# Performance work log

Hardware: AMD Instinct MI355X
Metric: run time of the kernel (lower is better)

The kernel has to match this reference:

```python
import jax, jax.numpy as jnp
import numpy as np

B, S, D, H, DK = 2, 2048, 1024, 16, 64  # d_model = n_heads * d_k

def setup_inputs() -> dict:
    key = jax.random.key(0)
    ks = jax.random.split(key, 11)
    s = 1.0 / np.sqrt(D)
    return {
        "Q": jax.random.normal(ks[0], (B, S, D), jnp.float32),
        "K": jax.random.normal(ks[1], (B, S, D), jnp.float32),
        "V": jax.random.normal(ks[2], (B, S, D), jnp.float32),
        "wq": jax.random.normal(ks[3], (D, D), jnp.float32) * s,
        "bq": jnp.zeros((D,), jnp.float32),
        "wk": jax.random.normal(ks[4], (D, D), jnp.float32) * s,
        "bk": jnp.zeros((D,), jnp.float32),
        "wv": jax.random.normal(ks[5], (D, D), jnp.float32) * s,
        "bv": jnp.zeros((D,), jnp.float32),
        "wo": jax.random.normal(ks[6], (D, D), jnp.float32) * s,
        "bo": jnp.zeros((D,), jnp.float32),
    }

def reference(Q, K, V, wq, bq, wk, bk, wv, bv, wo, bo):
    # linear projections (torch Linear: x @ W^T + b)
    q = Q @ wq.T + bq
    k = K @ wk.T + bk
    v = V @ wv.T + bv
    # split heads -> [B, H, S, DK]
    def split(t):
        return t.reshape(B, S, H, DK).transpose(0, 2, 1, 3)
    q, k, v = split(q), split(k), split(v)
    scale = 1.0 / np.sqrt(DK)
    scores = jnp.einsum('bhqd,bhkd->bhqk', q, k) * scale  # [B,H,S,S]
    probs = jax.nn.softmax(scores, axis=-1)
    # dropout is identity in eval mode
    ctx = jnp.einsum('bhqk,bhkd->bhqd', probs, v)  # [B,H,S,DK]
    ctx = ctx.transpose(0, 2, 1, 3).reshape(B, S, D)
    return ctx @ wo.T + bo
```

## Files before the change

kernel.cpp:

```cpp
#include <hip/hip_runtime.h>

#define S_LEN 2048
#define DMODEL 1024
#define DHEAD 64

typedef _Float16 half8 __attribute__((ext_vector_type(8)));
typedef _Float16 half4 __attribute__((ext_vector_type(4)));
typedef float f32x4 __attribute__((ext_vector_type(4)));
typedef int i32x4 __attribute__((ext_vector_type(4)));

#define LOG2E 1.4426950408889634f

__device__ __forceinline__ void async_copy16(const void* g, void* l) {
  __builtin_amdgcn_global_load_lds((__attribute__((address_space(1))) const void*)g,
                                   (__attribute__((address_space(3))) void*)l,
                                   16, 0, 0);
}

__device__ __forceinline__ void stage16_cvt(const float* __restrict__ gp, _Float16* lp) {
  float4 f0 = ((const float4*)gp)[0];
  float4 f1 = ((const float4*)gp)[1];
  float4 f2 = ((const float4*)gp)[2];
  float4 f3 = ((const float4*)gp)[3];
  half8 h0, h1;
  h0[0] = (_Float16)f0.x; h0[1] = (_Float16)f0.y; h0[2] = (_Float16)f0.z; h0[3] = (_Float16)f0.w;
  h0[4] = (_Float16)f1.x; h0[5] = (_Float16)f1.y; h0[6] = (_Float16)f1.z; h0[7] = (_Float16)f1.w;
  h1[0] = (_Float16)f2.x; h1[1] = (_Float16)f2.y; h1[2] = (_Float16)f2.z; h1[3] = (_Float16)f2.w;
  h1[4] = (_Float16)f3.x; h1[5] = (_Float16)f3.y; h1[6] = (_Float16)f3.z; h1[7] = (_Float16)f3.w;
  *(half8*)lp = h0;
  *(half8*)(lp + 8) = h1;
}

__global__ __launch_bounds__(256) void convert_w(const float* __restrict__ wq,
                                                 const float* __restrict__ wk,
                                                 const float* __restrict__ wv,
                                                 _Float16* __restrict__ dst) {
  const float* src = (blockIdx.y == 0) ? wq : (blockIdx.y == 1) ? wk : wv;
  _Float16* d = dst + (size_t)blockIdx.y * (DMODEL * DMODEL);
  int i = (blockIdx.x * 256 + threadIdx.x) * 4;
  float4 v = *(const float4*)(src + i);
  half4 h;
  h[0] = (_Float16)v.x; h[1] = (_Float16)v.y;
  h[2] = (_Float16)v.z; h[3] = (_Float16)v.w;
  *(half4*)(d + i) = h;
}

__global__ __launch_bounds__(256) void convert_wo(const float* __restrict__ wo,
                                                  _Float16* __restrict__ dst) {
  int i = (blockIdx.x * 256 + threadIdx.x) * 4;
  float4 v = *(const float4*)(wo + i);
  half4 h;
  h[0] = (_Float16)v.x; h[1] = (_Float16)v.y;
  h[2] = (_Float16)v.z; h[3] = (_Float16)v.w;
  *(half4*)(dst + i) = h;
}

__global__ __launch_bounds__(256) void qkv_gemm(
    const float* __restrict__ Qf, const float* __restrict__ Kf, const float* __restrict__ Vf,
    const _Float16* __restrict__ wh,
    const float* __restrict__ bq, const float* __restrict__ bk, const float* __restrict__ bv,
    _Float16* __restrict__ qo, _Float16* __restrict__ ko, _Float16* __restrict__ vt) {
  __shared__ __align__(16) _Float16 As[128 * 32];
  __shared__ __align__(16) _Float16 Bs[128 * 32];
  const int tid = threadIdx.x;
  const int wave = tid >> 6, lane = tid & 63;
  const int m15 = lane & 15, quad = lane >> 4;
  const int m0 = blockIdx.x * 128;
  const int gn0 = blockIdx.y * 128;
  const int sel = gn0 >> 10;
  const int n0 = gn0 & 1023;
  const float* Ag = (sel == 0) ? Qf : (sel == 1) ? Kf : Vf;
  const _Float16* Wg = wh + (size_t)sel * (DMODEL * DMODEL);
  const float* bias = (sel == 0) ? bq : (sel == 1) ? bk : bv;

  const int wm = (wave & 1) * 64, wn = (wave >> 1) * 64;
  const int sr = tid >> 1, sc16 = (tid & 1) * 16;

  f32x4 acc[4][4];
#pragma unroll
  for (int i = 0; i < 4; i++)
#pragma unroll
    for (int j = 0; j < 4; j++) {
      f32x4 z = {0.f, 0.f, 0.f, 0.f};
      acc[i][j] = z;
    }

  for (int k0 = 0; k0 < DMODEL; k0 += 32) {
#pragma unroll
    for (int p = 0; p < 2; p++) {
      int e = p * 2048 + tid * 8;
      async_copy16(Wg + (size_t)(n0 + (e >> 5)) * DMODEL + k0 + (e & 31),
                   (char*)Bs + p * 4096 + wave * 1024);
    }
    stage16_cvt(Ag + (size_t)(m0 + sr) * DMODEL + k0 + sc16, &As[sr * 32 + sc16]);
    __syncthreads();
    half8 af[4], bf[4];
#pragma unroll
    for (int i = 0; i < 4; i++)
      af[i] = *(const half8*)&As[(wm + i * 16 + m15) * 32 + quad * 8];
#pragma unroll
    for (int j = 0; j < 4; j++)
      bf[j] = *(const half8*)&Bs[(wn + j * 16 + m15) * 32 + quad * 8];
#pragma unroll
    for (int i = 0; i < 4; i++)
#pragma unroll
      for (int j = 0; j < 4; j++)
        acc[i][j] = __builtin_amdgcn_mfma_f32_16x16x32_f16(af[i], bf[j], acc[i][j], 0, 0, 0);
    __syncthreads();
  }
  if (sel != 2) {
    _Float16* outp = (sel == 0) ? qo : ko;
    const float scale = (sel == 0) ? (0.125f * LOG2E) : 1.0f;
#pragma unroll
    for (int i = 0; i < 4; i++) {
#pragma unroll
      for (int j = 0; j < 4; j++) {
        int gn = n0 + wn + j * 16 + m15;
        float bb = bias[gn];
#pragma unroll
        for (int r = 0; r < 4; r++) {
          int gm = m0 + wm + i * 16 + quad * 4 + r;
          outp[(size_t)gm * DMODEL + gn] = (_Float16)((acc[i][j][r] + bb) * scale);
        }
      }
    }
  } else {
#pragma unroll
    for (int i = 0; i < 4; i++) {
      int gm0 = m0 + wm + i * 16 + quad * 4;
      int b = gm0 >> 11, s = gm0 & 2047;
#pragma unroll
      for (int j = 0; j < 4; j++) {
        int gn = n0 + wn + j * 16 + m15;
        int h = gn >> 6, dk = gn & 63;
        float bb = bias[gn];
        half4 hv;
        hv[0] = (_Float16)(acc[i][j][0] + bb);
        hv[1] = (_Float16)(acc[i][j][1] + bb);
        hv[2] = (_Float16)(acc[i][j][2] + bb);
        hv[3] = (_Float16)(acc[i][j][3] + bb);
        *(half4*)(vt + ((size_t)(b * 16 + h) * 64 + dk) * 2048 + s) = hv;
      }
    }
  }
}

__global__ __launch_bounds__(256) void attn_kernel(const _Float16* __restrict__ qh,
                                                   const _Float16* __restrict__ kh,
                                                   const _Float16* __restrict__ vt,
                                                   _Float16* __restrict__ ctx) {
  __shared__ __align__(16) _Float16 Ks[2][64 * 64];
  __shared__ __align__(16) _Float16 Vs[2][64 * 64];
  const int tid = threadIdx.x;
  const int wave = tid >> 6, lane = tid & 63;
  const int m15 = lane & 15, qd = lane >> 4;
  const int q0 = blockIdx.x * 64;
  const int h = blockIdx.y, b = blockIdx.z;
  const size_t base = (size_t)b * S_LEN * DMODEL + (size_t)h * DHEAD;
  const size_t vbase = (size_t)(b * 16 + h) * 64 * 2048;

  const int qrow = q0 + wave * 16 + m15;
  half8 qf0 = *(const half8*)(qh + base + (size_t)qrow * DMODEL + qd * 8);
  half8 qf1 = *(const half8*)(qh + base + (size_t)qrow * DMODEL + 32 + qd * 8);

  const int l8 = lane >> 3, s8 = lane & 7;
  const int swz = (s8 ^ l8) * 8;
  const _Float16* ksrc = kh + base + (size_t)(wave * 8 + l8) * DMODEL + swz;
  const _Float16* vsrc = vt + vbase + (size_t)(wave * 8 + l8) * S_LEN + swz;
  char* kdst = (char*)&Ks[0][0] + wave * 1024;
  char* vdst = (char*)&Vs[0][0] + wave * 1024;

  const int kcol0 = ((qd ^ (m15 & 7)) << 4);

  f32x4 acc[4];
#pragma unroll
  for (int i = 0; i < 4; i++) { f32x4 z = {0.f, 0.f, 0.f, 0.f}; acc[i] = z; }
  float lsum = 0.f;

#pragma unroll
  for (int p = 0; p < 2; p++) {
    async_copy16(ksrc + (size_t)(p * 32) * DMODEL, kdst + p * 4096);
    async_copy16(vsrc + (size_t)(p * 32) * S_LEN, vdst + p * 4096);
  }
  __syncthreads();

  for (int it = 0; it < 32; it++) {
    const int buf = it & 1;
    if (it < 31) {
      const int kv = (it + 1) * 64;
#pragma unroll
      for (int p = 0; p < 2; p++) {
        async_copy16(ksrc + (size_t)(kv + p * 32) * DMODEL, kdst + (buf ^ 1) * 8192 + p * 4096);
        async_copy16(vsrc + (size_t)(p * 32) * S_LEN + kv, vdst + (buf ^ 1) * 8192 + p * 4096);
      }
    }
    const char* kb = (const char*)&Ks[buf][0];
    const char* vb = (const char*)&Vs[buf][0];

    f32x4 sc[4];
#pragma unroll
    for (int t = 0; t < 4; t++) {
      half8 kf0 = *(const half8*)(kb + (t * 16 + m15) * 128 + kcol0);
      half8 kf1 = *(const half8*)(kb + (t * 16 + m15) * 128 + (kcol0 ^ 64));
      f32x4 z = {0.f, 0.f, 0.f, 0.f};
      sc[t] = __builtin_amdgcn_mfma_f32_16x16x32_f16(kf0, qf0, z, 0, 0, 0);
      sc[t] = __builtin_amdgcn_mfma_f32_16x16x32_f16(kf1, qf1, sc[t], 0, 0, 0);
    }

    int pk[4][2];
#pragma unroll
    for (int t = 0; t < 4; t++) {
      float e0 = exp2f(sc[t][0]);
      float e1 = exp2f(sc[t][1]);
      float e2 = exp2f(sc[t][2]);
      float e3 = exp2f(sc[t][3]);
      lsum += (e0 + e1) + (e2 + e3);
      pk[t][0] = __builtin_bit_cast(int, __builtin_amdgcn_cvt_pkrtz(e0, e1));
      pk[t][1] = __builtin_bit_cast(int, __builtin_amdgcn_cvt_pkrtz(e2, e3));
    }

    i32x4 fh[2];
#pragma unroll
    for (int t1 = 0; t1 < 2; t1++) {
#pragma unroll
      for (int p = 0; p < 2; p++) {
        auto s1 = __builtin_amdgcn_permlane32_swap(pk[2 * t1][p], pk[2 * t1 + 1][p], false, false);
        auto s2 = __builtin_amdgcn_permlane16_swap(s1[0], s1[1], false, false);
        fh[t1][p] = (int)s2[0];
        fh[t1][2 + p] = (int)s2[1];
      }
    }
    half8 pA = __builtin_bit_cast(half8, fh[0]);
    half8 pB = __builtin_bit_cast(half8, fh[1]);

#pragma unroll
    for (int td = 0; td < 4; td++) {
      half8 vf0 = *(const half8*)(vb + (td * 16 + m15) * 128 + kcol0);
      half8 vf1 = *(const half8*)(vb + (td * 16 + m15) * 128 + (kcol0 ^ 64));
      acc[td] = __builtin_amdgcn_mfma_f32_16x16x32_f16(vf0, pA, acc[td], 0, 0, 0);
      acc[td] = __builtin_amdgcn_mfma_f32_16x16x32_f16(vf1, pB, acc[td], 0, 0, 0);
    }
    __syncthreads();
  }

  lsum += __shfl_xor(lsum, 16);
  lsum += __shfl_xor(lsum, 32);
  const float inv = 1.0f / lsum;

#pragma unroll
  for (int td = 0; td < 4; td++) {
    half4 hv;
#pragma unroll
    for (int r = 0; r < 4; r++) hv[r] = (_Float16)(acc[td][r] * inv);
    *(half4*)(ctx + base + (size_t)qrow * DMODEL + td * 16 + qd * 4) = hv;
  }
}

__global__ __launch_bounds__(256) void out_gemm(const _Float16* __restrict__ ch,
                                                const _Float16* __restrict__ who,
                                                const float* __restrict__ bo,
                                                float* __restrict__ out) {
  __shared__ __align__(16) _Float16 As[128 * 32];
  __shared__ __align__(16) _Float16 Bs[128 * 32];
  const int tid = threadIdx.x;
  const int wave = tid >> 6, lane = tid & 63;
  const int m15 = lane & 15, quad = lane >> 4;
  const int m0 = blockIdx.x * 128, n0 = blockIdx.y * 128;
  const int wm = (wave & 1) * 64, wn = (wave >> 1) * 64;

  f32x4 acc[4][4];
#pragma unroll
  for (int i = 0; i < 4; i++)
#pragma unroll
    for (int j = 0; j < 4; j++) {
      f32x4 z = {0.f, 0.f, 0.f, 0.f};
      acc[i][j] = z;
    }

  for (int k0 = 0; k0 < DMODEL; k0 += 32) {
#pragma unroll
    for (int p = 0; p < 2; p++) {
      int e = p * 2048 + tid * 8;
      async_copy16(ch + (size_t)(m0 + (e >> 5)) * DMODEL + k0 + (e & 31),
                   (char*)As + p * 4096 + wave * 1024);
      async_copy16(who + (size_t)(n0 + (e >> 5)) * DMODEL + k0 + (e & 31),
                   (char*)Bs + p * 4096 + wave * 1024);
    }
    __syncthreads();
    half8 af[4], bf[4];
#pragma unroll
    for (int i = 0; i < 4; i++)
      af[i] = *(const half8*)&As[(wm + i * 16 + m15) * 32 + quad * 8];
#pragma unroll
    for (int j = 0; j < 4; j++)
      bf[j] = *(const half8*)&Bs[(wn + j * 16 + m15) * 32 + quad * 8];
#pragma unroll
    for (int i = 0; i < 4; i++)
#pragma unroll
      for (int j = 0; j < 4; j++)
        acc[i][j] = __builtin_amdgcn_mfma_f32_16x16x32_f16(af[i], bf[j], acc[i][j], 0, 0, 0);
    __syncthreads();
  }
#pragma unroll
  for (int i = 0; i < 4; i++) {
#pragma unroll
    for (int j = 0; j < 4; j++) {
      int gn = n0 + wn + j * 16 + m15;
      float bb = bo[gn];
#pragma unroll
      for (int r = 0; r < 4; r++) {
        int gm = m0 + wm + i * 16 + quad * 4 + r;
        out[(size_t)gm * DMODEL + gn] = acc[i][j][r] + bb;
      }
    }
  }
}

extern "C" void kernel_launch(void* const* d_in, const int* in_sizes, int n_in,
                              void* d_out, int out_size, void* d_ws, size_t ws_size,
                              hipStream_t stream) {
  (void)in_sizes; (void)n_in; (void)out_size; (void)ws_size;
  const float* Q  = (const float*)d_in[0];
  const float* K  = (const float*)d_in[1];
  const float* V  = (const float*)d_in[2];
  const float* wq = (const float*)d_in[3];
  const float* bq = (const float*)d_in[4];
  const float* wk = (const float*)d_in[5];
  const float* bk = (const float*)d_in[6];
  const float* wv = (const float*)d_in[7];
  const float* bv = (const float*)d_in[8];
  const float* wo = (const float*)d_in[9];
  const float* bo = (const float*)d_in[10];
  float* out = (float*)d_out;

  _Float16* qh = (_Float16*)d_out;
  _Float16* kh = qh + (size_t)4194304;
  _Float16* vt = (_Float16*)d_ws;
  _Float16* wh = vt + (size_t)4194304;
  _Float16* ch = vt + (size_t)4194304;
  _Float16* who = (_Float16*)d_ws;

  convert_w<<<dim3(1024, 3), 256, 0, stream>>>(wq, wk, wv, wh);
  qkv_gemm<<<dim3(32, 24), 256, 0, stream>>>(Q, K, V, wh, bq, bk, bv, qh, kh, vt);
  attn_kernel<<<dim3(32, 16, 2), 256, 0, stream>>>(qh, kh, vt, ch);
  convert_wo<<<dim3(1024), 256, 0, stream>>>(wo, who);
  out_gemm<<<dim3(32, 8), 256, 0, stream>>>(ch, who, bo, out);
}
```

Baseline: 258.8 us.

## Split attention KV tile across waves instead of query rows, reduce via LDS

The attention kernel now has each wave own 16 keys of every 64-key tile across all 64 query rows, rather than owning 16 query rows across all keys. Each wave reads one K fragment per tile and uses 16x16x16 MFMAs for the PV product on locally produced probabilities. This removes the permlane shuffles and cuts redundant K/V LDS reads. The cost is a serialized cross-wave reduction of partial outputs and row sums through shared memory, with four barriers at the end, plus four times the accumulator registers. It also switches to the raw exp2 builtin.

```diff
diff --git a/kernel.cpp b/kernel.cpp
--- a/kernel.cpp
+++ b/kernel.cpp
@@ -7,7 +7,7 @@
 typedef _Float16 half8 __attribute__((ext_vector_type(8)));
 typedef _Float16 half4 __attribute__((ext_vector_type(4)));
 typedef float f32x4 __attribute__((ext_vector_type(4)));
-typedef int i32x4 __attribute__((ext_vector_type(4)));
+typedef int i32x2 __attribute__((ext_vector_type(2)));
 
 #define LOG2E 1.4426950408889634f
 
@@ -149,8 +149,7 @@
                                                    const _Float16* __restrict__ kh,
                                                    const _Float16* __restrict__ vt,
                                                    _Float16* __restrict__ ctx) {
-  __shared__ __align__(16) _Float16 Ks[2][64 * 64];
-  __shared__ __align__(16) _Float16 Vs[2][64 * 64];
+  __shared__ __align__(16) char smem[32768];
   const int tid = threadIdx.x;
   const int wave = tid >> 6, lane = tid & 63;
   const int m15 = lane & 15, qd = lane >> 4;
@@ -159,23 +158,30 @@
   const size_t base = (size_t)b * S_LEN * DMODEL + (size_t)h * DHEAD;
   const size_t vbase = (size_t)(b * 16 + h) * 64 * 2048;
 
-  const int qrow = q0 + wave * 16 + m15;
-  half8 qf0 = *(const half8*)(qh + base + (size_t)qrow * DMODEL + qd * 8);
-  half8 qf1 = *(const half8*)(qh + base + (size_t)qrow * DMODEL + 32 + qd * 8);
+  half8 qf[4][2];
+#pragma unroll
+  for (int qt = 0; qt < 4; qt++) {
+    const _Float16* qp = qh + base + (size_t)(q0 + qt * 16 + m15) * DMODEL + qd * 8;
+    qf[qt][0] = *(const half8*)qp;
+    qf[qt][1] = *(const half8*)(qp + 32);
+  }
 
   const int l8 = lane >> 3, s8 = lane & 7;
   const int swz = (s8 ^ l8) * 8;
   const _Float16* ksrc = kh + base + (size_t)(wave * 8 + l8) * DMODEL + swz;
   const _Float16* vsrc = vt + vbase + (size_t)(wave * 8 + l8) * S_LEN + swz;
-  char* kdst = (char*)&Ks[0][0] + wave * 1024;
-  char* vdst = (char*)&Vs[0][0] + wave * 1024;
+  char* kdst = smem + wave * 1024;
+  char* vdst = smem + 16384 + wave * 1024;
 
   const int kcol0 = ((qd ^ (m15 & 7)) << 4);
-
-  f32x4 acc[4];
-#pragma unroll
-  for (int i = 0; i < 4; i++) { f32x4 z = {0.f, 0.f, 0.f, 0.f}; acc[i] = z; }
-  float lsum = 0.f;
+  const int vcol = ((((wave * 2 + (qd >> 1)) ^ (m15 & 7)) << 4) + (qd & 1) * 8);
+
+  f32x4 acc[4][4];
+#pragma unroll
+  for (int i = 0; i < 4; i++)
+#pragma unroll
+    for (int j = 0; j < 4; j++) { f32x4 z = {0.f, 0.f, 0.f, 0.f}; acc[i][j] = z; }
+  float ls[4] = {0.f, 0.f, 0.f, 0.f};
 
 #pragma unroll
   for (int p = 0; p < 2; p++) {
@@ -194,65 +200,86 @@
         async_copy16(vsrc + (size_t)(p * 32) * S_LEN + kv, vdst + (buf ^ 1) * 8192 + p * 4096);
       }
     }
-    const char* kb = (const char*)&Ks[buf][0];
-    const char* vb = (const char*)&Vs[buf][0];
+    const char* kb = smem + buf * 8192;
+    const char* vb = smem + 16384 + buf * 8192;
+
+    half8 kf0 = *(const half8*)(kb + (wave * 16 + m15) * 128 + kcol0);
+    half8 kf1 = *(const half8*)(kb + (wave * 16 + m15) * 128 + (kcol0 ^ 64));
 
     f32x4 sc[4];
 #pragma unroll
-    for (int t = 0; t < 4; t++) {
-      half8 kf0 = *(const half8*)(kb + (t * 16 + m15) * 128 + kcol0);
-      half8 kf1 = *(const half8*)(kb + (t * 16 + m15) * 128 + (kcol0 ^ 64));
+    for (int qt = 0; qt < 4; qt++) {
       f32x4 z = {0.f, 0.f, 0.f, 0.f};
-      sc[t] = __builtin_amdgcn_mfma_f32_16x16x32_f16(kf0, qf0, z, 0, 0, 0);
-      sc[t] = __builtin_amdgcn_mfma_f32_16x16x32_f16(kf1, qf1, sc[t], 0, 0, 0);
-    }
-
-    int pk[4][2];
-#pragma unroll
-    for (int t = 0; t < 4; t++) {
-      float e0 = exp2f(sc[t][0]);
-      float e1 = exp2f(sc[t][1]);
-      float e2 = exp2f(sc[t][2]);
-      float e3 = exp2f(sc[t][3]);
-      lsum += (e0 + e1) + (e2 + e3);
-      pk[t][0] = __builtin_bit_cast(int, __builtin_amdgcn_cvt_pkrtz(e0, e1));
-      pk[t][1] = __builtin_bit_cast(int, __builtin_amdgcn_cvt_pkrtz(e2, e3));
-    }
-
-    i32x4 fh[2];
-#pragma unroll
-    for (int t1 = 0; t1 < 2; t1++) {
-#pragma unroll
-      for (int p = 0; p < 2; p++) {
-        auto s1 = __builtin_amdgcn_permlane32_swap(pk[2 * t1][p], pk[2 * t1 + 1][p], false, false);
-        auto s2 = __builtin_amdgcn_permlane16_swap(s1[0], s1[1], false, false);
-        fh[t1][p] = (int)s2[0];
-        fh[t1][2 + p] = (int)s2[1];
-      }
-    }
-    half8 pA = __builtin_bit_cast(half8, fh[0]);
-    half8 pB = __builtin_bit_cast(half8, fh[1]);
+      sc[qt] = __builtin_amdgcn_mfma_f32_16x16x32_f16(kf0, qf[qt][0], z, 0, 0, 0);
+      sc[qt] = __builtin_amdgcn_mfma_f32_16x16x32_f16(kf1, qf[qt][1], sc[qt], 0, 0, 0);
+    }
+
+    half4 p[4];
+#pragma unroll
+    for (int qt = 0; qt < 4; qt++) {
+      float e0 = __builtin_amdgcn_exp2f(sc[qt][0]);
+      float e1 = __builtin_amdgcn_exp2f(sc[qt][1]);
+      float e2 = __builtin_amdgcn_exp2f(sc[qt][2]);
+      float e3 = __builtin_amdgcn_exp2f(sc[qt][3]);
+      ls[qt] += (e0 + e1) + (e2 + e3);
+      i32x2 w2;
+      w2[0] = __builtin_bit_cast(int, __builtin_amdgcn_cvt_pkrtz(e0, e1));
+      w2[1] = __builtin_bit_cast(int, __builtin_amdgcn_cvt_pkrtz(e2, e3));
+      p[qt] = __builtin_bit_cast(half4, w2);
+    }
 
 #pragma unroll
     for (int td = 0; td < 4; td++) {
-      half8 vf0 = *(const half8*)(vb + (td * 16 + m15) * 128 + kcol0);
-      half8 vf1 = *(const half8*)(vb + (td * 16 + m15) * 128 + (kcol0 ^ 64));
-      acc[td] = __builtin_amdgcn_mfma_f32_16x16x32_f16(vf0, pA, acc[td], 0, 0, 0);
-      acc[td] = __builtin_amdgcn_mfma_f32_16x16x32_f16(vf1, pB, acc[td], 0, 0, 0);
-    }
-    __syncthreads();
-  }
-
-  lsum += __shfl_xor(lsum, 16);
-  lsum += __shfl_xor(lsum, 32);
-  const float inv = 1.0f / lsum;
-
-#pragma unroll
-  for (int td = 0; td < 4; td++) {
-    half4 hv;
-#pragma unroll
-    for (int r = 0; r < 4; r++) hv[r] = (_Float16)(acc[td][r] * inv);
-    *(half4*)(ctx + base + (size_t)qrow * DMODEL + td * 16 + qd * 4) = hv;
+      half4 vf = *(const half4*)(vb + (td * 16 + m15) * 128 + vcol);
+#pragma unroll
+      for (int qt = 0; qt < 4; qt++)
+        acc[td][qt] = __builtin_amdgcn_mfma_f32_16x16x16f16(vf, p[qt], acc[td][qt], 0, 0, 0);
+    }
+    __syncthreads();
+  }
+
+  float* Ored = (float*)smem;
+  float* Lred = (float*)(smem + 17408);
+
+#pragma unroll
+  for (int qt = 0; qt < 4; qt++) {
+    ls[qt] += __shfl_xor(ls[qt], 16);
+    ls[qt] += __shfl_xor(ls[qt], 32);
+  }
+  if (qd == 0) {
+#pragma unroll
+    for (int qt = 0; qt < 4; qt++) Lred[wave * 64 + qt * 16 + m15] = ls[qt];
+  }
+
+  for (int w = 0; w < 4; w++) {
+    if (wave == w) {
+#pragma unroll
+      for (int td = 0; td < 4; td++)
+#pragma unroll
+        for (int qt = 0; qt < 4; qt++)
+#pragma unroll
+          for (int r = 0; r < 4; r++) {
+            int addr = (qt * 16 + m15) * 65 + td * 16 + qd * 4 + r;
+            if (w == 0) Ored[addr] = acc[td][qt][r];
+            else        Ored[addr] += acc[td][qt][r];
+          }
+    }
+    __syncthreads();
+  }
+
+  {
+    const int q = wave * 16 + (lane >> 2);
+    const int dc = (lane & 3) * 16;
+    const float inv = 1.0f / (Lred[q] + Lred[64 + q] + Lred[128 + q] + Lred[192 + q]);
+    const float* rp = Ored + q * 65 + dc;
+    half8 h0, h1;
+#pragma unroll
+    for (int j = 0; j < 8; j++) h0[j] = (_Float16)(rp[j] * inv);
+#pragma unroll
+    for (int j = 0; j < 8; j++) h1[j] = (_Float16)(rp[8 + j] * inv);
+    _Float16* op = ctx + base + (size_t)(q0 + q) * DMODEL + dc;
+    *(half8*)op = h0;
+    *(half8*)(op + 8) = h1;
   }
 }
 
```

Result: no change. 261.1 us (+0.9%).
